# Kernel tuning notes

Hardware: AMD Instinct MI355X
Metric: run time of the kernel (lower is better)

Reference implementation:

```python
import jax, jax.numpy as jnp
import numpy as np
from jax import lax

B, C, H, W = 2, 128, 128, 128
Hs, Ws = 64, 64
DG, KK = 8, 9          # deformable groups, kernel positions (3x3)
CG = C // DG           # channels per deformable group = 16
COUT = C // 2          # dcn output channels = 64


def setup_inputs() -> dict:
    key = jax.random.key(0)
    ks = jax.random.split(key, 9)
    s = 0.05
    return {
        "feat_l": jax.random.normal(ks[0], (B, C, H, W), jnp.float32),
        "feat_s": jax.random.normal(ks[1], (B, C, Hs, Ws), jnp.float32),
        "fsm_w": jax.random.normal(ks[2], (C, C, 1, 1), jnp.float32) * s,
        "offset_w": jax.random.normal(ks[3], (C, 2 * C, 1, 1), jnp.float32) * s,
        "com_w": jax.random.normal(ks[4], (3 * DG * KK, C, 3, 3), jnp.float32) * s,
        "com_b": jax.random.normal(ks[5], (3 * DG * KK,), jnp.float32) * s,
        "dcn_w": jax.random.normal(ks[6], (COUT, C, 3, 3), jnp.float32) * s,
        "dcn_b": jax.random.normal(ks[7], (COUT,), jnp.float32) * s,
        "cat_w": jax.random.normal(ks[8], (C, COUT, 1, 1), jnp.float32) * s,
    }


def _conv(x, w, pad):
    return lax.conv_general_dilated(x, w, (1, 1), [(pad, pad), (pad, pad)],
                                    dimension_numbers=("NCHW", "OIHW", "NCHW"))


def _bilinear(feat_g, py, px):
    # feat_g: [B,DG,CG,H,W]; py/px: [B,DG,KK,H,W] fractional sample coords.
    Hf, Wf = feat_g.shape[-2], feat_g.shape[-1]
    y0 = jnp.floor(py)
    x0 = jnp.floor(px)
    ly = py - y0
    lx = px - x0
    y0i = y0.astype(jnp.int32)
    x0i = x0.astype(jnp.int32)
    flat = feat_g.reshape(B, DG, 1, CG, Hf * Wf)  # broadcast over KK

    def gather(yi, xi, wgt):
        valid = ((yi >= 0) & (yi < Hf) & (xi >= 0) & (xi < Wf)).astype(feat_g.dtype)
        idx = (jnp.clip(yi, 0, Hf - 1) * Wf + jnp.clip(xi, 0, Wf - 1))
        idx = idx.reshape(B, DG, KK, 1, H * W)
        v = jnp.take_along_axis(flat, idx, axis=-1)  # [B,DG,KK,CG,H*W]
        return v * (wgt * valid).reshape(B, DG, KK, 1, H * W)

    acc = (gather(y0i, x0i, (1 - ly) * (1 - lx))
           + gather(y0i, x0i + 1, (1 - ly) * lx)
           + gather(y0i + 1, x0i, ly * (1 - lx))
           + gather(y0i + 1, x0i + 1, ly * lx))
    return acc.reshape(B, DG, KK, CG, H, W)


def reference(feat_l, feat_s, fsm_w, offset_w, com_w, com_b, dcn_w, dcn_b, cat_w):
    # nearest-neighbor upsample of feat_s to feat_l's HxW (F.interpolate nearest)
    idx_h = (jnp.arange(H) * Hs) // H
    idx_w = (jnp.arange(W) * Ws) // W
    feat_up = feat_s[:, :, idx_h][:, :, :, idx_w]

    feat_arm = jax.nn.relu(_conv(feat_l, fsm_w, 0))                       # FSM (1x1 conv+relu)
    off_feat = jax.nn.relu(_conv(jnp.concatenate([feat_arm, feat_up * 2], axis=1), offset_w, 0))

    # DCNv2 pack: 3x3 conv -> (o1, o2, mask)
    om = _conv(off_feat, com_w, 1) + com_b[None, :, None, None]
    o1, o2, m = jnp.split(om, 3, axis=1)
    offset = jnp.concatenate([o1, o2], axis=1).reshape(B, DG, KK, 2, H, W)  # (y,x) per (g,pos)
    mask = jax.nn.sigmoid(m).reshape(B, DG, KK, H, W)

    # sampling coords: p + kernel offset + learned offset (stride=1, pad=1, dil=1)
    kyy = (jnp.arange(KK) // 3 - 1).astype(jnp.float32)
    kxx = (jnp.arange(KK) % 3 - 1).astype(jnp.float32)
    py = (jnp.arange(H, dtype=jnp.float32)[None, None, None, :, None]
          + kyy[None, None, :, None, None] + offset[:, :, :, 0])
    px = (jnp.arange(W, dtype=jnp.float32)[None, None, None, None, :]
          + kxx[None, None, :, None, None] + offset[:, :, :, 1])

    feat_g = feat_up.reshape(B, DG, CG, H, W)
    val = _bilinear(feat_g, py, px) * mask[:, :, :, None]  # [B,DG,KK,CG,H,W]

    w_r = dcn_w.reshape(COUT, DG, CG, KK)
    out = jnp.einsum('bgkchw,ogck->bohw', val, w_r) + dcn_b[None, :, None, None]
    feat_align = jax.nn.relu(out)

    return jax.nn.relu(_conv(feat_align, cat_w, 0)) + feat_arm
```

## Files before the change

### kernel.cpp

```cpp
#include <hip/hip_runtime.h>
#include <cstdint>
#include <cstddef>


typedef _Float16 f16x8 __attribute__((ext_vector_type(8)));
typedef _Float16 f16x4 __attribute__((ext_vector_type(4)));
typedef float    f32x4 __attribute__((ext_vector_type(4)));

__device__ __forceinline__ float relu_(float x) { return fmaxf(x, 0.f); }

template<int MODE, int CIN>
__global__ __launch_bounds__(256) void conv1x1_kernel(
    const float* __restrict__ in1, const float* __restrict__ in2,
    const float* __restrict__ Wm, float* __restrict__ out)
{
  constexpr int IN1C = (MODE == 2) ? 64 : 128;
  const int b  = blockIdx.y;
  const int p0 = blockIdx.x * 64;
  const int tid = threadIdx.x;
  const int tx = tid & 7;
  const int ty = tid >> 3;

  __shared__ float Xs[16][64];
  __shared__ float Wt[16][128];

  float acc[4][8];
#pragma unroll
  for (int i = 0; i < 4; ++i)
#pragma unroll
    for (int j = 0; j < 8; ++j) acc[i][j] = 0.f;

  const int cS  = tid >> 4;
  const int pxS = (tid & 15) * 4;
  const int ocS = (tid & 15) * 8;

  for (int cc = 0; cc < CIN; cc += 16) {
    __syncthreads();
    {
      int gc = cc + cS;
      float4 v;
      if (MODE == 1 && gc >= 128) {
        int sc = gc - 128;
        float t[4];
#pragma unroll
        for (int j = 0; j < 4; ++j) {
          int pp = p0 + pxS + j;
          int hh = pp >> 7, ww = pp & 127;
          t[j] = 2.f * in2[((size_t)(b * 128 + sc) << 12) + ((hh >> 1) << 6) + (ww >> 1)];
        }
        v = make_float4(t[0], t[1], t[2], t[3]);
      } else {
        v = *(const float4*)(in1 + ((size_t)(b * IN1C + gc) << 14) + p0 + pxS);
      }
      *(float4*)&Xs[cS][pxS] = v;
#pragma unroll
      for (int j = 0; j < 8; ++j)
        Wt[cS][ocS + j] = Wm[(ocS + j) * CIN + cc + cS];
    }
    __syncthreads();
#pragma unroll
    for (int c = 0; c < 16; ++c) {
      float4 wv = *(const float4*)&Wt[c][ty * 4];
      float4 x0 = *(const float4*)&Xs[c][tx * 8];
      float4 x1 = *(const float4*)&Xs[c][tx * 8 + 4];
      float xs[8] = {x0.x, x0.y, x0.z, x0.w, x1.x, x1.y, x1.z, x1.w};
      float wf[4] = {wv.x, wv.y, wv.z, wv.w};
#pragma unroll
      for (int i = 0; i < 4; ++i)
#pragma unroll
        for (int j = 0; j < 8; ++j)
          acc[i][j] = fmaf(wf[i], xs[j], acc[i][j]);
    }
  }

#pragma unroll
  for (int i = 0; i < 4; ++i) {
    int oc = ty * 4 + i;
    size_t base = ((size_t)(b * 128 + oc) << 14) + p0 + tx * 8;
    float r[8];
#pragma unroll
    for (int j = 0; j < 8; ++j) r[j] = relu_(acc[i][j]);
    if (MODE == 2) {
#pragma unroll
      for (int j = 0; j < 8; ++j) r[j] += in2[base + j];
    }
    *(float4*)(out + base)     = make_float4(r[0], r[1], r[2], r[3]);
    *(float4*)(out + base + 4) = make_float4(r[4], r[5], r[6], r[7]);
  }
}

__global__ __launch_bounds__(256) void t2h2_kernel(
    const float* __restrict__ fl, const float* __restrict__ fs,
    _Float16* __restrict__ flTh, _Float16* __restrict__ fsTh)
{
  const int bx = blockIdx.x;
  const float* src;
  _Float16* dst;
  int HW, p0;
  if (bx < 512) { src = fl; dst = flTh; HW = 16384; p0 = bx * 32; }
  else          { src = fs; dst = fsTh; HW = 4096;  p0 = (bx - 512) * 32; }
  const int b  = blockIdx.z;
  const int c0 = blockIdx.y * 32;
  const int tid = threadIdx.x;
  __shared__ float T[32][33];
  {
    int pxl = tid & 31, cy = tid >> 5;
#pragma unroll
    for (int j = 0; j < 4; ++j) {
      int c = cy + j * 8;
      T[c][pxl] = src[((size_t)(b * 128 + c0 + c)) * HW + p0 + pxl];
    }
  }
  __syncthreads();
  {
    int cq = tid & 7, pr = tid >> 3;
    f16x4 v;
#pragma unroll
    for (int e = 0; e < 4; ++e) v[e] = (_Float16)T[cq * 4 + e][pr];
    *(f16x4*)&dst[(((size_t)b * HW) + p0 + pr) * 128 + c0 + cq * 4] = v;
  }
}

__global__ __launch_bounds__(256) void wfall_kernel(
    const float* __restrict__ fsm_w, const float* __restrict__ offset_w,
    const float* __restrict__ com_w, const float* __restrict__ dcn_w,
    const float* __restrict__ cat_w,
    _Float16* __restrict__ WfA, _Float16* __restrict__ WfB,
    _Float16* __restrict__ WfP, _Float16* __restrict__ Wf2,
    _Float16* __restrict__ WfC)
{
  const int bid = blockIdx.x;
  if (bid < 8) {
    int idx = bid * 256 + threadIdx.x;
    int lane = idx & 63;
    int t = idx >> 6;
    int m = t & 7, q = t >> 3;
    int oc = m * 16 + (lane & 15);
    int c0 = q * 32 + (lane >> 4) * 8;
    f16x8 v;
#pragma unroll
    for (int j = 0; j < 8; ++j) v[j] = (_Float16)fsm_w[oc * 128 + c0 + j];
    ((f16x8*)WfA)[idx] = v;
  } else if (bid < 24) {
    int idx = (bid - 8) * 256 + threadIdx.x;
    int lane = idx & 63;
    int t = idx >> 6;
    int m = t & 7, q = t >> 3;
    int oc = m * 16 + (lane & 15);
    int c0 = q * 32 + (lane >> 4) * 8;
    float s = (q >= 4) ? 2.f : 1.f;
    f16x8 v;
#pragma unroll
    for (int j = 0; j < 8; ++j) v[j] = (_Float16)(offset_w[oc * 256 + c0 + j] * s);
    ((f16x8*)WfB)[idx] = v;
  } else if (bid < 168) {
    int idx = (bid - 24) * 256 + threadIdx.x;
    int lane = idx & 63;
    int t = idx >> 6;
    int m = t & 7;
    int t2 = t >> 3;
    int half = t2 & 1, q = t2 >> 1;
    int kk = q >> 2;
    int ic0 = (q & 3) * 32 + (lane >> 4) * 8;
    int oc = half * 128 + m * 16 + (lane & 15);
    f16x8 v;
#pragma unroll
    for (int j = 0; j < 8; ++j) {
      float x = (oc < 216) ? com_w[((size_t)oc * 128 + ic0 + j) * 9 + kk] : 0.f;
      v[j] = (_Float16)x;
    }
    ((f16x8*)WfP)[idx] = v;
  } else if (bid < 204) {
    int idx = (bid - 168) * 256 + threadIdx.x;
    int lane = idx & 63;
    int t = idx >> 6;
    int m = t & 3, q = t >> 2;
    int oc = m * 16 + (lane & 15);
    f16x8 v;
#pragma unroll
    for (int j = 0; j < 8; ++j) {
      int rp = q * 32 + (lane >> 4) * 8 + j;
      int c = rp & 15, tt = rp >> 4;
      int g = tt / 9, k = tt % 9;
      v[j] = (_Float16)dcn_w[((size_t)oc * 128 + g * 16 + c) * 9 + k];
    }
    ((f16x8*)Wf2)[idx] = v;
  } else {
    int idx = (bid - 204) * 256 + threadIdx.x;
    int lane = idx & 63;
    int t = idx >> 6;
    int m = t & 7, q = t >> 3;
    int oc = m * 16 + (lane & 15);
    int k0 = q * 32 + (lane >> 4) * 8;
    f16x8 v;
#pragma unroll
    for (int j = 0; j < 8; ++j) v[j] = (_Float16)cat_w[oc * 64 + k0 + j];
    ((f16x8*)WfC)[idx] = v;
  }
}

__global__ __launch_bounds__(256) void fsm_gemm_kernel(
    const _Float16* __restrict__ flTh, const _Float16* __restrict__ WfA,
    float* __restrict__ arm, _Float16* __restrict__ armh)
{
  const int b    = blockIdx.y;
  const int tid  = threadIdx.x;
  const int wv   = tid >> 6;
  const int lane = tid & 63;
  const int px0  = blockIdx.x * 64 + wv * 16;
  const int pxl  = px0 + (lane & 15);

  f32x4 acc[8];
#pragma unroll
  for (int m = 0; m < 8; ++m) acc[m] = (f32x4){0.f, 0.f, 0.f, 0.f};

  const f16x8* Bp = (const f16x8*)flTh + (((size_t)b << 14) + pxl) * 16 + (lane >> 4);
  const f16x8* Ap = (const f16x8*)WfA + lane;

#pragma unroll
  for (int q = 0; q < 4; ++q) {
    f16x8 bf = Bp[q * 4];
#pragma unroll
    for (int m = 0; m < 8; ++m)
      acc[m] = __builtin_amdgcn_mfma_f32_16x16x32_f16(Ap[(q * 8 + m) * 64], bf, acc[m], 0, 0, 0);
  }

  const int r0 = (lane >> 4) * 4;
#pragma unroll
  for (int m = 0; m < 8; ++m) {
    f16x4 h;
#pragma unroll
    for (int r = 0; r < 4; ++r) {
      float v = relu_(acc[m][r]);
      arm[((size_t)(b * 128 + m * 16 + r0 + r) << 14) + pxl] = v;
      h[r] = (_Float16)v;
    }
    *(f16x4*)&armh[(((size_t)b << 14) + pxl) * 128 + m * 16 + r0] = h;
  }
}

__global__ __launch_bounds__(256) void off_gemm_kernel(
    const _Float16* __restrict__ armh, const _Float16* __restrict__ fsTh,
    const _Float16* __restrict__ WfB, _Float16* __restrict__ offh)
{
  const int b    = blockIdx.y;
  const int tid  = threadIdx.x;
  const int wv   = tid >> 6;
  const int lane = tid & 63;
  const int px0  = blockIdx.x * 64 + wv * 16;
  const int pxl  = px0 + (lane & 15);
  const int h = pxl >> 7, w = pxl & 127;
  const int pup = ((h >> 1) << 6) + (w >> 1);

  f32x4 acc[8];
#pragma unroll
  for (int m = 0; m < 8; ++m) acc[m] = (f32x4){0.f, 0.f, 0.f, 0.f};

  const f16x8* BpA = (const f16x8*)armh + (((size_t)b << 14) + pxl) * 16 + (lane >> 4);
  const f16x8* BpU = (const f16x8*)fsTh + (((size_t)b << 12) + pup) * 16 + (lane >> 4);
  const f16x8* Ap  = (const f16x8*)WfB + lane;

#pragma unroll
  for (int q = 0; q < 8; ++q) {
    f16x8 bf = (q < 4) ? BpA[q * 4] : BpU[(q - 4) * 4];
#pragma unroll
    for (int m = 0; m < 8; ++m)
      acc[m] = __builtin_amdgcn_mfma_f32_16x16x32_f16(Ap[(q * 8 + m) * 64], bf, acc[m], 0, 0, 0);
  }

  const int r0 = (lane >> 4) * 4;
#pragma unroll
  for (int m = 0; m < 8; ++m) {
    f16x4 hh;
#pragma unroll
    for (int r = 0; r < 4; ++r) hh[r] = (_Float16)relu_(acc[m][r]);
    *(f16x4*)&offh[(((size_t)b << 14) + pxl) * 128 + m * 16 + r0] = hh;
  }
}

__global__ __launch_bounds__(256) void com_gemm_kernel(
    const _Float16* __restrict__ offh, const _Float16* __restrict__ WfP,
    const float* __restrict__ cb, float* __restrict__ om)
{
  const int b    = blockIdx.z;
  const int half = blockIdx.y;
  const int tid  = threadIdx.x;
  const int lane = tid & 63;
  const int px0  = blockIdx.x * 64 + (tid >> 6) * 16;
  const int pxl  = px0 + (lane & 15);
  const int h = pxl >> 7, w = pxl & 127;

  __shared__ f16x8 As[512];

  f32x4 acc[8];
#pragma unroll
  for (int m = 0; m < 8; ++m) acc[m] = (f32x4){0.f, 0.f, 0.f, 0.f};

  const f16x8* Bbase = (const f16x8*)offh + ((size_t)b << 14) * 16 + (lane >> 4);
  const f16x8* Wp    = (const f16x8*)WfP + half * 512 + tid * 2;
  const f16x8 zero = {(_Float16)0.f, (_Float16)0.f, (_Float16)0.f, (_Float16)0.f,
                      (_Float16)0.f, (_Float16)0.f, (_Float16)0.f, (_Float16)0.f};

  auto loadB = [&](int t) -> f16x8 {
    const int kk = t >> 2, ic4 = t & 3;
    const int hh = h + kk / 3 - 1;
    const int ww = w + kk % 3 - 1;
    const bool valid = ((unsigned)hh < 128u) && ((unsigned)ww < 128u);
    const int ps = valid ? ((hh << 7) + ww) : 0;
    f16x8 bf = Bbase[(size_t)ps * 16 + ic4 * 4];
    return valid ? bf : zero;
  };

  f16x8 rA0 = Wp[0], rA1 = Wp[1];
  f16x8 bfA = loadB(0), bfB = loadB(1);

#pragma unroll 1
  for (int tt = 0; tt < 18; ++tt) {
    const int t0 = tt * 2;
    __syncthreads();
    As[tid * 2] = rA0; As[tid * 2 + 1] = rA1;
    __syncthreads();
    rA0 = Wp[(t0 + 1) * 1024]; rA1 = Wp[(t0 + 1) * 1024 + 1];
    {
      f16x8 bu = bfA;
      if (t0 + 2 < 36) bfA = loadB(t0 + 2);
#pragma unroll
      for (int m = 0; m < 8; ++m)
        acc[m] = __builtin_amdgcn_mfma_f32_16x16x32_f16(As[m * 64 + lane], bu, acc[m], 0, 0, 0);
    }
    __syncthreads();
    As[tid * 2] = rA0; As[tid * 2 + 1] = rA1;
    __syncthreads();
    if (t0 + 2 < 36) { rA0 = Wp[(t0 + 2) * 1024]; rA1 = Wp[(t0 + 2) * 1024 + 1]; }
    {
      f16x8 bu = bfB;
      if (t0 + 3 < 36) bfB = loadB(t0 + 3);
#pragma unroll
      for (int m = 0; m < 8; ++m)
        acc[m] = __builtin_amdgcn_mfma_f32_16x16x32_f16(As[m * 64 + lane], bu, acc[m], 0, 0, 0);
    }
  }

  const int r0i = (lane >> 4) * 4;
#pragma unroll
  for (int m = 0; m < 8; ++m) {
#pragma unroll
    for (int r = 0; r < 4; ++r) {
      int oc = half * 128 + m * 16 + r0i + r;
      if (oc < 216)
        om[((size_t)(b * 216 + oc) << 14) + pxl] = acc[m][r] + cb[oc];
    }
  }
}

__global__ __launch_bounds__(256) void sample_kernel(
    const _Float16* __restrict__ fsTh, const float* __restrict__ om,
    _Float16* __restrict__ valh)
{
  const int idx = blockIdx.x * 256 + threadIdx.x;
  const int px4 = (idx & 4095) << 2;
  const int t  = idx >> 12;
  const int k  = t % 9;
  const int g  = (t / 9) & 7;
  const int b  = t / 72;

  const size_t omb = ((size_t)b * 216) << 14;
  const float4 oy4 = *(const float4*)(om + omb + ((size_t)(g * 18 + 2 * k) << 14) + px4);
  const float4 ox4 = *(const float4*)(om + omb + ((size_t)(g * 18 + 2 * k + 1) << 14) + px4);
  const float4 mr4 = *(const float4*)(om + omb + ((size_t)(144 + g * 9 + k) << 14) + px4);
  const float oys[4] = {oy4.x, oy4.y, oy4.z, oy4.w};
  const float oxs[4] = {ox4.x, ox4.y, ox4.z, ox4.w};
  const float mrs[4] = {mr4.x, mr4.y, mr4.z, mr4.w};

  const _Float16* fb = fsTh + ((size_t)b << 19);
  const int t9 = g * 9 + k;
  _Float16* dstb = valh + (((size_t)(b * 36 + (t9 >> 1)) * 16384 + px4) * 32 + (t9 & 1) * 16);

  const int kdy = k / 3 - 1, kdx = k % 3 - 1;
  const int h = px4 >> 7, w0 = px4 & 127;
  const int gbase = g * 16;

#pragma unroll
  for (int i = 0; i < 4; ++i) {
    const float mv = 1.f / (1.f + __expf(-mrs[i]));
    const float py  = (float)(h + kdy) + oys[i];
    const float pxx = (float)(w0 + i + kdx) + oxs[i];
    const float y0f = floorf(py), x0f = floorf(pxx);
    const float ly = py - y0f, lx = pxx - x0f;
    const int y0 = (int)y0f, x0i = (int)x0f;
    const int y1 = y0 + 1, x1 = x0i + 1;

    const int y0c = min(max(y0, 0), 127), y1c = min(max(y1, 0), 127);
    const int x0c = min(max(x0i, 0), 127), x1c = min(max(x1, 0), 127);

    float w00 = (1.f - ly) * (1.f - lx) * mv;
    float w01 = (1.f - ly) * lx * mv;
    float w10 = ly * (1.f - lx) * mv;
    float w11 = ly * lx * mv;
    const bool vy0 = (unsigned)y0 < 128u, vy1 = (unsigned)y1 < 128u;
    const bool vx0 = (unsigned)x0i < 128u, vx1 = (unsigned)x1 < 128u;
    w00 = (vy0 && vx0) ? w00 : 0.f;
    w01 = (vy0 && vx1) ? w01 : 0.f;
    w10 = (vy1 && vx0) ? w10 : 0.f;
    w11 = (vy1 && vx1) ? w11 : 0.f;

    const int a00 = ((((y0c >> 1) << 6) + (x0c >> 1)) << 7) + gbase;
    const int a01 = ((((y0c >> 1) << 6) + (x1c >> 1)) << 7) + gbase;
    const int a10 = ((((y1c >> 1) << 6) + (x0c >> 1)) << 7) + gbase;
    const int a11 = ((((y1c >> 1) << 6) + (x1c >> 1)) << 7) + gbase;

    f16x8 t00a = *(const f16x8*)(fb + a00), t00b = *(const f16x8*)(fb + a00 + 8);
    f16x8 t01a = *(const f16x8*)(fb + a01), t01b = *(const f16x8*)(fb + a01 + 8);
    f16x8 t10a = *(const f16x8*)(fb + a10), t10b = *(const f16x8*)(fb + a10 + 8);
    f16x8 t11a = *(const f16x8*)(fb + a11), t11b = *(const f16x8*)(fb + a11 + 8);

    f16x8 ov0, ov1;
#pragma unroll
    for (int j = 0; j < 8; ++j) {
      ov0[j] = (_Float16)(w00 * (float)t00a[j] + w01 * (float)t01a[j]
                        + w10 * (float)t10a[j] + w11 * (float)t11a[j]);
      ov1[j] = (_Float16)(w00 * (float)t00b[j] + w01 * (float)t01b[j]
                        + w10 * (float)t10b[j] + w11 * (float)t11b[j]);
    }

    _Float16* dst = dstb + i * 32;
    ((f16x8*)dst)[0] = ov0;
    ((f16x8*)dst)[1] = ov1;
  }
}

__global__ __launch_bounds__(256) void dcn_gemm_kernel(
    const _Float16* __restrict__ valh, const _Float16* __restrict__ Wf2,
    const float* __restrict__ db, _Float16* __restrict__ alh)
{
  const int b    = blockIdx.y;
  const int tid  = threadIdx.x;
  const int wv   = tid >> 6;
  const int lane = tid & 63;
  const int px0  = blockIdx.x * 64 + wv * 16;

  f32x4 acc[4];
#pragma unroll
  for (int m = 0; m < 4; ++m) acc[m] = (f32x4){0.f, 0.f, 0.f, 0.f};

  const f16x8* Bp = (const f16x8*)valh
      + ((size_t)(b * 36) * 16384 + px0 + (lane & 15)) * 4 + (lane >> 4);
  const f16x8* Ap = (const f16x8*)Wf2 + lane;

#pragma unroll 2
  for (int q = 0; q < 36; ++q) {
    f16x8 bf = Bp[(size_t)q * 65536];
    const f16x8* ap = Ap + q * 256;
#pragma unroll
    for (int m = 0; m < 4; ++m)
      acc[m] = __builtin_amdgcn_mfma_f32_16x16x32_f16(ap[m * 64], bf, acc[m], 0, 0, 0);
  }

  const int pxl = px0 + (lane & 15);
  const int r0  = (lane >> 4) * 4;
#pragma unroll
  for (int m = 0; m < 4; ++m) {
    f16x4 hv;
#pragma unroll
    for (int r = 0; r < 4; ++r) {
      int oc = m * 16 + r0 + r;
      hv[r] = (_Float16)relu_(acc[m][r] + db[oc]);
    }
    *(f16x4*)&alh[(((size_t)b << 14) + pxl) * 64 + m * 16 + r0] = hv;
  }
}

__global__ __launch_bounds__(256) void cat_gemm_kernel(
    const _Float16* __restrict__ alh, const _Float16* __restrict__ WfC,
    const float* __restrict__ arm, float* __restrict__ out)
{
  const int b    = blockIdx.y;
  const int tid  = threadIdx.x;
  const int wv   = tid >> 6;
  const int lane = tid & 63;
  const int px0  = blockIdx.x * 64 + wv * 16;
  const int pxl  = px0 + (lane & 15);

  f32x4 acc[8];
#pragma unroll
  for (int m = 0; m < 8; ++m) acc[m] = (f32x4){0.f, 0.f, 0.f, 0.f};

  const f16x8* Bp = (const f16x8*)alh + (((size_t)b << 14) + pxl) * 8 + (lane >> 4);
  const f16x8* Ap = (const f16x8*)WfC + lane;

#pragma unroll
  for (int q = 0; q < 2; ++q) {
    f16x8 bf = Bp[q * 4];
#pragma unroll
    for (int m = 0; m < 8; ++m)
      acc[m] = __builtin_amdgcn_mfma_f32_16x16x32_f16(Ap[(q * 8 + m) * 64], bf, acc[m], 0, 0, 0);
  }

  const int r0 = (lane >> 4) * 4;
#pragma unroll
  for (int m = 0; m < 8; ++m) {
#pragma unroll
    for (int r = 0; r < 4; ++r) {
      int oc = m * 16 + r0 + r;
      size_t a = ((size_t)(b * 128 + oc) << 14) + pxl;
      out[a] = relu_(acc[m][r]) + arm[a];
    }
  }
}

__global__ __launch_bounds__(256) void com_conv_kernel(
    const float* __restrict__ x, const float* __restrict__ cw,
    const float* __restrict__ cb, float* __restrict__ om)
{
  const int b    = blockIdx.z;
  const int ocg  = blockIdx.y;
  const int tile = blockIdx.x;
  const int th = (tile >> 2) * 32, tw = (tile & 3) * 32;
  const int tid = threadIdx.x;
  const int lw = (tid & 7) * 4;
  const int lh = tid >> 3;

  __shared__ float Xs[8 * 34 * 34];

  float acc[8][4];
#pragma unroll
  for (int a = 0; a < 8; ++a)
#pragma unroll
    for (int p = 0; p < 4; ++p) acc[a][p] = 0.f;

  for (int cc = 0; cc < 128; cc += 8) {
    __syncthreads();
    for (int idx = tid; idx < 8 * 1156; idx += 256) {
      int ic  = idx / 1156;
      int rem = idx - ic * 1156;
      int yy  = rem / 34;
      int xx  = rem - yy * 34;
      int gh = th + yy - 1, gw = tw + xx - 1;
      float v = 0.f;
      if ((unsigned)gh < 128u && (unsigned)gw < 128u)
        v = x[((size_t)(b * 128 + cc + ic) << 14) + (gh << 7) + gw];
      Xs[idx] = v;
    }
    __syncthreads();
#pragma unroll 1
    for (int ic = 0; ic < 8; ++ic) {
      float xr[3][6];
#pragma unroll
      for (int ky = 0; ky < 3; ++ky)
#pragma unroll
        for (int xx = 0; xx < 6; ++xx)
          xr[ky][xx] = Xs[ic * 1156 + (lh + ky) * 34 + lw + xx];
      const float* wp = cw + ((size_t)(ocg * 8) * 128 + (cc + ic)) * 9;
#pragma unroll
      for (int a = 0; a < 8; ++a) {
        const float* w9 = wp + a * 1152;
#pragma unroll
        for (int ky = 0; ky < 3; ++ky)
#pragma unroll
          for (int kx = 0; kx < 3; ++kx) {
            float wv = w9[ky * 3 + kx];
#pragma unroll
            for (int p = 0; p < 4; ++p)
              acc[a][p] = fmaf(wv, xr[ky][kx + p], acc[a][p]);
          }
      }
    }
  }

#pragma unroll
  for (int a = 0; a < 8; ++a) {
    int oc = ocg * 8 + a;
    float bv = cb[oc];
    float4 r = make_float4(acc[a][0] + bv, acc[a][1] + bv,
                           acc[a][2] + bv, acc[a][3] + bv);
    *(float4*)(om + ((size_t)(b * 216 + oc) << 14) + ((th + lh) << 7) + tw + lw) = r;
  }
}

__global__ __launch_bounds__(256) void wt_kernel(const float* __restrict__ dw,
                                                 float* __restrict__ wT)
{
  int idx = blockIdx.x * 256 + threadIdx.x;
  int o    = idx & 63;
  int rest = idx >> 6;
  int k    = rest % 9;
  int gc   = rest / 9;
  wT[idx] = dw[(o * 128 + gc) * 9 + k];
}

__global__ __launch_bounds__(256) void dcn_kernel(
    const float* __restrict__ fs, const float* __restrict__ om,
    const float* __restrict__ wT, const float* __restrict__ db,
    float* __restrict__ al)
{
  const int b   = blockIdx.y;
  const int p0  = blockIdx.x * 32;
  const int tid = threadIdx.x;
  const int px  = tid & 31;
  const int g   = tid >> 5;
  const int p = p0 + px;
  const int h = p >> 7, w = p & 127;

  float acc[64];
#pragma unroll
  for (int o = 0; o < 64; ++o) acc[o] = 0.f;

  const size_t omb = ((size_t)b * 216) << 14;
  const float* fsg = fs + (((size_t)(b * 128 + g * 16)) << 12);
  const float* wg  = wT + g * (16 * 9 * 64);

#pragma unroll 1
  for (int k = 0; k < 9; ++k) {
    float offy = om[omb + ((size_t)(g * 18 + 2 * k) << 14) + p];
    float offx = om[omb + ((size_t)(g * 18 + 2 * k + 1) << 14) + p];
    float mraw = om[omb + ((size_t)(144 + g * 9 + k) << 14) + p];
    float mv = 1.f / (1.f + __expf(-mraw));

    float py  = (float)(h + k / 3 - 1) + offy;
    float pxx = (float)(w + k % 3 - 1) + offx;
    float y0f = floorf(py), x0f = floorf(pxx);
    float ly = py - y0f, lx = pxx - x0f;
    int y0 = (int)y0f, x0i = (int)x0f;
    int y1 = y0 + 1, x1 = x0i + 1;

    int y0c = min(max(y0, 0), 127), y1c = min(max(y1, 0), 127);
    int x0c = min(max(x0i, 0), 127), x1c = min(max(x1, 0), 127);
    int ry0 = (y0c >> 1) << 6, ry1 = (y1c >> 1) << 6;
    int cx0 = x0c >> 1, cx1 = x1c >> 1;

    float w00 = (1.f - ly) * (1.f - lx) * mv;
    float w01 = (1.f - ly) * lx * mv;
    float w10 = ly * (1.f - lx) * mv;
    float w11 = ly * lx * mv;
    bool vy0 = (unsigned)y0 < 128u, vy1 = (unsigned)y1 < 128u;
    bool vx0 = (unsigned)x0i < 128u, vx1 = (unsigned)x1 < 128u;
    w00 = (vy0 && vx0) ? w00 : 0.f;
    w01 = (vy0 && vx1) ? w01 : 0.f;
    w10 = (vy1 && vx0) ? w10 : 0.f;
    w11 = (vy1 && vx1) ? w11 : 0.f;

#pragma unroll 1
    for (int c = 0; c < 16; ++c) {
      const float* fc = fsg + (c << 12);
      float v00 = fc[ry0 + cx0];
      float v01 = fc[ry0 + cx1];
      float v10 = fc[ry1 + cx0];
      float v11 = fc[ry1 + cx1];
      float v = w00 * v00 + w01 * v01 + w10 * v10 + w11 * v11;
      const float* wp = wg + (c * 9 + k) * 64;
#pragma unroll
      for (int oq = 0; oq < 16; ++oq) {
        float4 w4 = *(const float4*)(wp + oq * 4);
        acc[oq * 4 + 0] = fmaf(v, w4.x, acc[oq * 4 + 0]);
        acc[oq * 4 + 1] = fmaf(v, w4.y, acc[oq * 4 + 1]);
        acc[oq * 4 + 2] = fmaf(v, w4.z, acc[oq * 4 + 2]);
        acc[oq * 4 + 3] = fmaf(v, w4.w, acc[oq * 4 + 3]);
      }
    }
  }

  __shared__ float red[256][17];
  const int px2 = tid & 31;
  const int og  = tid >> 5;
#pragma unroll
  for (int r = 0; r < 4; ++r) {
    __syncthreads();
#pragma unroll
    for (int j = 0; j < 16; ++j) red[tid][j] = acc[r * 16 + j];
    __syncthreads();
#pragma unroll
    for (int jj = 0; jj < 2; ++jj) {
      int ol = og * 2 + jj;
      float s = 0.f;
#pragma unroll
      for (int gg = 0; gg < 8; ++gg) s += red[gg * 32 + px2][ol];
      int oc = r * 16 + ol;
      s += db[oc];
      al[((size_t)(b * 64 + oc) << 14) + p0 + px2] = fmaxf(s, 0.f);
    }
  }
}

extern "C" void kernel_launch(void* const* d_in, const int* in_sizes, int n_in,
                              void* d_out, int out_size, void* d_ws, size_t ws_size,
                              hipStream_t stream)
{
  const float* feat_l   = (const float*)d_in[0];
  const float* feat_s   = (const float*)d_in[1];
  const float* fsm_w    = (const float*)d_in[2];
  const float* offset_w = (const float*)d_in[3];
  const float* com_w    = (const float*)d_in[4];
  const float* com_b    = (const float*)d_in[5];
  const float* dcn_w    = (const float*)d_in[6];
  const float* dcn_b    = (const float*)d_in[7];
  const float* cat_w    = (const float*)d_in[8];
  float* out = (float*)d_out;
  float* ws  = (float*)d_ws;

  const size_t NEED = (size_t)(4194304 + 7077888 + 2097152 + 1048576 + 37748736) * 4;

  if (ws_size >= NEED) {
    float* arm      = ws;
    float* om       = ws + 4194304;
    _Float16* alh   = (_Float16*)(ws + 11272192);
    _Float16* Wf2   = (_Float16*)(ws + 12320768);
    _Float16* WfC   = (_Float16*)(ws + 12357632);
    _Float16* fsTh  = (_Float16*)(ws + 13369344);
    _Float16* flTh  = (_Float16*)(ws + 13893632);
    _Float16* armh  = (_Float16*)(ws + 15990784);
    _Float16* offh  = (_Float16*)(ws + 18087936);
    _Float16* valh  = (_Float16*)(ws + 20185088);
    _Float16* WfA   = (_Float16*)(ws + 39059456);
    _Float16* WfB   = (_Float16*)(ws + 39067648);
    _Float16* WfP   = (_Float16*)(ws + 39084032);

    hipLaunchKernelGGL(wfall_kernel, dim3(208), dim3(256), 0, stream,
                       fsm_w, offset_w, com_w, dcn_w, cat_w, WfA, WfB, WfP, Wf2, WfC);
    hipLaunchKernelGGL(t2h2_kernel, dim3(640, 4, 2), dim3(256), 0, stream,
                       feat_l, feat_s, flTh, fsTh);
    hipLaunchKernelGGL(fsm_gemm_kernel, dim3(256, 2), dim3(256), 0, stream,
                       flTh, WfA, arm, armh);
    hipLaunchKernelGGL(off_gemm_kernel, dim3(256, 2), dim3(256), 0, stream,
                       armh, fsTh, WfB, offh);
    hipLaunchKernelGGL(com_gemm_kernel, dim3(256, 2, 2), dim3(256), 0, stream,
                       offh, WfP, com_b, om);
    hipLaunchKernelGGL(sample_kernel, dim3(2304), dim3(256), 0, stream,
                       fsTh, om, valh);
    hipLaunchKernelGGL(dcn_gemm_kernel, dim3(256, 2), dim3(256), 0, stream,
                       valh, Wf2, dcn_b, alh);
    hipLaunchKernelGGL(cat_gemm_kernel, dim3(256, 2), dim3(256), 0, stream,
                       alh, WfC, arm, out);
  } else {
    float* arm = ws;
    float* off = ws + 4194304;
    float* om  = ws + 8388608;
    float* al  = ws + 15466496;
    float* wT  = ws + 17563648;

    hipLaunchKernelGGL(wt_kernel, dim3(288), dim3(256), 0, stream, dcn_w, wT);
    hipLaunchKernelGGL((conv1x1_kernel<0, 128>), dim3(256, 2), dim3(256), 0, stream,
                       feat_l, nullptr, fsm_w, arm);
    hipLaunchKernelGGL((conv1x1_kernel<1, 256>), dim3(256, 2), dim3(256), 0, stream,
                       arm, feat_s, offset_w, off);
    hipLaunchKernelGGL(com_conv_kernel, dim3(16, 27, 2), dim3(256), 0, stream,
                       off, com_w, com_b, om);
    hipLaunchKernelGGL(dcn_kernel, dim3(512, 2), dim3(256), 0, stream,
                       feat_s, om, wT, dcn_b, al);
    hipLaunchKernelGGL((conv1x1_kernel<2, 64>), dim3(256, 2), dim3(256), 0, stream,
                       al, arm, cat_w, out);
  }
}
```

Measured before the change: 225.6 us.

## Fuse deformable bilinear sampling into the DCN MFMA GEMM kernel

Merges the separate sampling kernel and the DCN GEMM into one kernel. Each lane computes its bilinearly sampled fp16 fragment in registers and feeds it straight into the MFMA, so the large intermediate value buffer is no longer written to and re-read from global memory. The cost is that each block now runs the offset reads, sigmoid and gather inside the GEMM loop with unroll 1. The fused grid is also much smaller than the old sampling grid, which may expose gather latency.

```diff
diff --git a/kernel.cpp b/kernel.cpp
--- a/kernel.cpp
+++ b/kernel.cpp
@@ -353,38 +353,42 @@
   }
 }
 
-__global__ __launch_bounds__(256) void sample_kernel(
+__global__ __launch_bounds__(256) void dcn_fused_kernel(
     const _Float16* __restrict__ fsTh, const float* __restrict__ om,
-    _Float16* __restrict__ valh)
-{
-  const int idx = blockIdx.x * 256 + threadIdx.x;
-  const int px4 = (idx & 4095) << 2;
-  const int t  = idx >> 12;
-  const int k  = t % 9;
-  const int g  = (t / 9) & 7;
-  const int b  = t / 72;
-
-  const size_t omb = ((size_t)b * 216) << 14;
-  const float4 oy4 = *(const float4*)(om + omb + ((size_t)(g * 18 + 2 * k) << 14) + px4);
-  const float4 ox4 = *(const float4*)(om + omb + ((size_t)(g * 18 + 2 * k + 1) << 14) + px4);
-  const float4 mr4 = *(const float4*)(om + omb + ((size_t)(144 + g * 9 + k) << 14) + px4);
-  const float oys[4] = {oy4.x, oy4.y, oy4.z, oy4.w};
-  const float oxs[4] = {ox4.x, ox4.y, ox4.z, ox4.w};
-  const float mrs[4] = {mr4.x, mr4.y, mr4.z, mr4.w};
-
+    const _Float16* __restrict__ Wf2, const float* __restrict__ db,
+    _Float16* __restrict__ alh)
+{
+  const int b    = blockIdx.y;
+  const int tid  = threadIdx.x;
+  const int wv   = tid >> 6;
+  const int lane = tid & 63;
+  const int px0  = blockIdx.x * 64 + wv * 16;
+  const int pxl  = px0 + (lane & 15);
+  const int h = pxl >> 7, w = pxl & 127;
+  const int t9add = lane >> 5;
+  const int chalf = ((lane >> 4) & 1) << 3;
+
+  const float* omp = om + (((size_t)b * 216) << 14) + pxl;
   const _Float16* fb = fsTh + ((size_t)b << 19);
-  const int t9 = g * 9 + k;
-  _Float16* dstb = valh + (((size_t)(b * 36 + (t9 >> 1)) * 16384 + px4) * 32 + (t9 & 1) * 16);
-
-  const int kdy = k / 3 - 1, kdx = k % 3 - 1;
-  const int h = px4 >> 7, w0 = px4 & 127;
-  const int gbase = g * 16;
-
-#pragma unroll
-  for (int i = 0; i < 4; ++i) {
-    const float mv = 1.f / (1.f + __expf(-mrs[i]));
-    const float py  = (float)(h + kdy) + oys[i];
-    const float pxx = (float)(w0 + i + kdx) + oxs[i];
+  const f16x8* Ap = (const f16x8*)Wf2 + lane;
+
+  f32x4 acc[4];
+#pragma unroll
+  for (int m = 0; m < 4; ++m) acc[m] = (f32x4){0.f, 0.f, 0.f, 0.f};
+
+#pragma unroll 1
+  for (int q = 0; q < 36; ++q) {
+    const int t9 = 2 * q + t9add;
+    const int g = t9 / 9;
+    const int k = t9 - g * 9;
+
+    const float offy = omp[(size_t)(g * 18 + 2 * k) << 14];
+    const float offx = omp[(size_t)(g * 18 + 2 * k + 1) << 14];
+    const float mraw = omp[(size_t)(144 + t9) << 14];
+    const float mv = 1.f / (1.f + __expf(-mraw));
+
+    const float py  = (float)(h + k / 3 - 1) + offy;
+    const float pxx = (float)(w + k % 3 - 1) + offx;
     const float y0f = floorf(py), x0f = floorf(pxx);
     const float ly = py - y0f, lx = pxx - x0f;
     const int y0 = (int)y0f, x0i = (int)x0f;
@@ -404,60 +408,30 @@
     w10 = (vy1 && vx0) ? w10 : 0.f;
     w11 = (vy1 && vx1) ? w11 : 0.f;
 
-    const int a00 = ((((y0c >> 1) << 6) + (x0c >> 1)) << 7) + gbase;
-    const int a01 = ((((y0c >> 1) << 6) + (x1c >> 1)) << 7) + gbase;
-    const int a10 = ((((y1c >> 1) << 6) + (x0c >> 1)) << 7) + gbase;
-    const int a11 = ((((y1c >> 1) << 6) + (x1c >> 1)) << 7) + gbase;
-
-    f16x8 t00a = *(const f16x8*)(fb + a00), t00b = *(const f16x8*)(fb + a00 + 8);
-    f16x8 t01a = *(const f16x8*)(fb + a01), t01b = *(const f16x8*)(fb + a01 + 8);
-    f16x8 t10a = *(const f16x8*)(fb + a10), t10b = *(const f16x8*)(fb + a10 + 8);
-    f16x8 t11a = *(const f16x8*)(fb + a11), t11b = *(const f16x8*)(fb + a11 + 8);
-
-    f16x8 ov0, ov1;
-#pragma unroll
-    for (int j = 0; j < 8; ++j) {
-      ov0[j] = (_Float16)(w00 * (float)t00a[j] + w01 * (float)t01a[j]
-                        + w10 * (float)t10a[j] + w11 * (float)t11a[j]);
-      ov1[j] = (_Float16)(w00 * (float)t00b[j] + w01 * (float)t01b[j]
-                        + w10 * (float)t10b[j] + w11 * (float)t11b[j]);
-    }
-
-    _Float16* dst = dstb + i * 32;
-    ((f16x8*)dst)[0] = ov0;
-    ((f16x8*)dst)[1] = ov1;
-  }
-}
-
-__global__ __launch_bounds__(256) void dcn_gemm_kernel(
-    const _Float16* __restrict__ valh, const _Float16* __restrict__ Wf2,
-    const float* __restrict__ db, _Float16* __restrict__ alh)
-{
-  const int b    = blockIdx.y;
-  const int tid  = threadIdx.x;
-  const int wv   = tid >> 6;
-  const int lane = tid & 63;
-  const int px0  = blockIdx.x * 64 + wv * 16;
-
-  f32x4 acc[4];
-#pragma unroll
-  for (int m = 0; m < 4; ++m) acc[m] = (f32x4){0.f, 0.f, 0.f, 0.f};
-
-  const f16x8* Bp = (const f16x8*)valh
-      + ((size_t)(b * 36) * 16384 + px0 + (lane & 15)) * 4 + (lane >> 4);
-  const f16x8* Ap = (const f16x8*)Wf2 + lane;
-
-#pragma unroll 2
-  for (int q = 0; q < 36; ++q) {
-    f16x8 bf = Bp[(size_t)q * 65536];
+    const int gb = g * 16 + chalf;
+    const int a00 = ((((y0c >> 1) << 6) + (x0c >> 1)) << 7) + gb;
+    const int a01 = ((((y0c >> 1) << 6) + (x1c >> 1)) << 7) + gb;
+    const int a10 = ((((y1c >> 1) << 6) + (x0c >> 1)) << 7) + gb;
+    const int a11 = ((((y1c >> 1) << 6) + (x1c >> 1)) << 7) + gb;
+
+    f16x8 t00 = *(const f16x8*)(fb + a00);
+    f16x8 t01 = *(const f16x8*)(fb + a01);
+    f16x8 t10 = *(const f16x8*)(fb + a10);
+    f16x8 t11 = *(const f16x8*)(fb + a11);
+
+    f16x8 bf;
+#pragma unroll
+    for (int j = 0; j < 8; ++j)
+      bf[j] = (_Float16)(w00 * (float)t00[j] + w01 * (float)t01[j]
+                       + w10 * (float)t10[j] + w11 * (float)t11[j]);
+
     const f16x8* ap = Ap + q * 256;
 #pragma unroll
     for (int m = 0; m < 4; ++m)
       acc[m] = __builtin_amdgcn_mfma_f32_16x16x32_f16(ap[m * 64], bf, acc[m], 0, 0, 0);
   }
 
-  const int pxl = px0 + (lane & 15);
-  const int r0  = (lane >> 4) * 4;
+  const int r0 = (lane >> 4) * 4;
 #pragma unroll
   for (int m = 0; m < 4; ++m) {
     f16x4 hv;
@@ -709,7 +683,6 @@
     _Float16* flTh  = (_Float16*)(ws + 13893632);
     _Float16* armh  = (_Float16*)(ws + 15990784);
     _Float16* offh  = (_Float16*)(ws + 18087936);
-    _Float16* valh  = (_Float16*)(ws + 20185088);
     _Float16* WfA   = (_Float16*)(ws + 39059456);
     _Float16* WfB   = (_Float16*)(ws + 39067648);
     _Float16* WfP   = (_Float16*)(ws + 39084032);
@@ -724,10 +697,8 @@
                        armh, fsTh, WfB, offh);
     hipLaunchKernelGGL(com_gemm_kernel, dim3(256, 2, 2), dim3(256), 0, stream,
                        offh, WfP, com_b, om);
-    hipLaunchKernelGGL(sample_kernel, dim3(2304), dim3(256), 0, stream,
-                       fsTh, om, valh);
-    hipLaunchKernelGGL(dcn_gemm_kernel, dim3(256, 2), dim3(256), 0, stream,
-                       valh, Wf2, dcn_b, alh);
+    hipLaunchKernelGGL(dcn_fused_kernel, dim3(256, 2), dim3(256), 0, stream,
+                       fsTh, om, Wf2, dcn_b, alh);
     hipLaunchKernelGGL(cat_gemm_kernel, dim3(256, 2), dim3(256), 0, stream,
                        alh, WfC, arm, out);
   } else {
```

Result: faster. 187.7 us (-16.8%).
